# Performance work log

Hardware: AMD Instinct MI355X
Metric: run time of the kernel (lower is better)

## Reference

```python
import jax, jax.numpy as jnp
import numpy as np


def setup_inputs() -> dict:
    key = jax.random.key(0)
    k1, k2, k3 = jax.random.split(key, 3)
    B, Cin, Cout, K, H, W = 4, 64, 64, 3, 160, 160
    inputs = jax.random.normal(k1, (B, Cin, H, W), dtype=jnp.float32)
    # fractional dilation rates in [1, 3]
    rate_map = 1.0 + 2.0 * jax.random.uniform(k2, (B, 1, H, W), dtype=jnp.float32)
    # xavier-uniform-ish init
    limit = float(np.sqrt(6.0 / (Cin * K * K + Cout * K * K)))
    weight = jax.random.uniform(k3, (Cout, Cin, K, K), dtype=jnp.float32,
                                minval=-limit, maxval=limit)
    bias = jnp.zeros((Cout,), dtype=jnp.float32)
    return {"inputs": inputs, "weight": weight, "rate_map": rate_map,
            "bias": bias, "stride_h": 1, "stride_w": 1}


def _pdconv2d(inputs, weight, rate_map, bias, stride_h, stride_w):
    """Perspective (fractional, per-pixel) dilated conv with same padding.

    For each output pixel, the KxK taps are placed at center + offset*rate,
    where rate comes from rate_map and may be fractional -> bilinear sampling
    with zeros outside the image.
    """
    B, C, H, W = inputs.shape
    O, _, K, _ = weight.shape
    HO = (H + stride_h - 1) // stride_h
    WO = (W + stride_w - 1) // stride_w

    rate = rate_map[:, 0, ::stride_h, ::stride_w]  # [B,HO,WO]
    cy = (jnp.arange(HO) * stride_h).astype(jnp.float32)
    cx = (jnp.arange(WO) * stride_w).astype(jnp.float32)
    off = jnp.arange(K, dtype=jnp.float32) - (K - 1) / 2.0  # centered taps

    # sampling coords [B,HO,WO,K,K]
    sy = cy[None, :, None, None, None] + off[None, None, None, :, None] * rate[:, :, :, None, None]
    sx = cx[None, None, :, None, None] + off[None, None, None, None, :] * rate[:, :, :, None, None]
    sy = jnp.broadcast_to(sy, (B, HO, WO, K, K))
    sx = jnpp = jnp.broadcast_to(sx, (B, HO, WO, K, K))
    sx = jnp_p = sx  # no-op alias (keeps names clear)

    y0 = jnp.floor(sy)
    x0 = jnp.floor(sx)
    wy = sy - y0  # bilinear weights
    wx = sx - x0
    y0i = y0.astype(jnp.int32)
    x0i = x0.astype(jnp.int32)

    img = inputs.reshape(B, C, H * W)

    def gather(idx):  # idx [B,HO,WO,K,K] -> [B,C,HO,WO,K,K]
        return jax.vmap(lambda im, ix: jnp.take(im, ix, axis=-1))(img, idx)

    acc = jnp.zeros((B, C, HO, WO, K, K), dtype=inputs.dtype)
    corners = [(0, 0, (1 - wy) * (1 - wx)), (0, 1, (1 - wy) * wx),
               (1, 0, wy * (1 - wx)), (1, 1, wy * wx)]
    for dy, dx, cw in corners:
        yy = y0i + dy
        xx = x0i + dx
        valid = (yy >= 0) & (yy < H) & (xx >= 0) & (xx < W)
        idx = jnp.clip(yy, 0, H - 1) * W + jnp.clip(xx, 0, W - 1)
        w = (cw * valid.astype(inputs.dtype))[:, None]  # [B,1,HO,WO,K,K]
        acc = acc + gather(idx) * w

    # [B,C,HO,WO,K,K] x [O,C,K,K] -> [B,O,HO,WO]
    out = jnp.einsum('bchwkl,ockl->bohw', acc, weight)
    return out + bias[None, :, None, None]


def reference(inputs, weight, rate_map, bias, stride_h, stride_w):
    return _pdconv2d(inputs, weight, rate_map, bias, stride_h, stride_w)
```

## Files before the change

kernel.cpp:

```cpp
#include <hip/hip_runtime.h>
#include <hip/hip_bf16.h>

#define NB   4
#define CIN  64
#define COUT 64
#define HH   160
#define WW   160
#define HW   (HH * WW)

#define RT   8
#define CT   22
#define RS   72
#define RSB  (RS * 2)
#define HIN_SHORTS (RT * CT * RS)

typedef __attribute__((ext_vector_type(8))) short bf16x8;
typedef __attribute__((ext_vector_type(4))) float f32x4;
typedef __attribute__((ext_vector_type(2))) float f32x2;
typedef __attribute__((ext_vector_type(4))) unsigned int u32x4;

static __device__ __forceinline__ short f2bf(float v) {
    return __builtin_bit_cast(short, __float2bfloat16(v));
}

__global__ void wtf_kernel(const float* __restrict__ w, short* __restrict__ wtf) {
    int i = blockIdx.x * 256 + threadIdx.x;
    if (i < 36864) {
        const int j  = i & 7;
        const int l  = (i >> 3) & 63;
        const int mt = (i >> 9) & 3;
        const int ks = (i >> 11) & 1;
        const int t  = i >> 12;
        const int o  = 16 * mt + (l & 15);
        const int c  = 32 * ks + 8 * (l >> 4) + j;
        wtf[i] = f2bf(w[(o * CIN + c) * 9 + t]);
    }
}

__global__ __launch_bounds__(256) void tin_kernel(const float* __restrict__ in,
                                                  short* __restrict__ tin) {
    const int cpx = gridDim.x >> 3;
    const int wb  = (blockIdx.x & 7) * cpx + (blockIdx.x >> 3);
    const int gid = wb * 256 + threadIdx.x;
    if (gid >= NB * HW) return;
    const int b  = gid / HW;
    const int hw = gid - b * HW;
    const float* src = in + (size_t)b * CIN * HW + hw;
    short* dst = tin + (size_t)gid * CIN;
#pragma unroll
    for (int chunk = 0; chunk < 4; ++chunk) {
        union { u32x4 v; short s[8]; } p0, p1;
#pragma unroll
        for (int cc = 0; cc < 8; ++cc)
            p0.s[cc] = f2bf(src[(size_t)(chunk * 16 + cc) * HW]);
#pragma unroll
        for (int cc = 0; cc < 8; ++cc)
            p1.s[cc] = f2bf(src[(size_t)(chunk * 16 + 8 + cc) * HW]);
        *(u32x4*)(dst + chunk * 16)     = p0.v;
        *(u32x4*)(dst + chunk * 16 + 8) = p1.v;
    }
}

static __device__ __forceinline__ void consume_tap(
    const u32x4 v00, const u32x4 v01, const u32x4 v10, const u32x4 v11,
    const float c00, const float c01, const float c10, const float c11,
    const bf16x8 wf0, const bf16x8 wf1, const bf16x8 wf2, const bf16x8 wf3,
    f32x4 acc[4])
{
    union { bf16x8 v; unsigned u[4]; } pf;
#pragma unroll
    for (int wd = 0; wd < 4; ++wd) {
        f32x2 s;
        {
            const unsigned u0 = v00[wd];
            const f32x2 xv = { __builtin_bit_cast(float, u0 << 16),
                               __builtin_bit_cast(float, u0 & 0xffff0000u) };
            s = c00 * xv;
        }
        {
            const unsigned u0 = v01[wd];
            const f32x2 xv = { __builtin_bit_cast(float, u0 << 16),
                               __builtin_bit_cast(float, u0 & 0xffff0000u) };
            s += c01 * xv;
        }
        {
            const unsigned u0 = v10[wd];
            const f32x2 xv = { __builtin_bit_cast(float, u0 << 16),
                               __builtin_bit_cast(float, u0 & 0xffff0000u) };
            s += c10 * xv;
        }
        {
            const unsigned u0 = v11[wd];
            const f32x2 xv = { __builtin_bit_cast(float, u0 << 16),
                               __builtin_bit_cast(float, u0 & 0xffff0000u) };
            s += c11 * xv;
        }
        unsigned r;
        asm("v_cvt_pk_bf16_f32 %0, %1, %2" : "=v"(r) : "v"(s.x), "v"(s.y));
        pf.u[wd] = r;
    }
    acc[0] = __builtin_amdgcn_mfma_f32_16x16x32_bf16(wf0, pf.v, acc[0], 0, 0, 0);
    acc[1] = __builtin_amdgcn_mfma_f32_16x16x32_bf16(wf1, pf.v, acc[1], 0, 0, 0);
    acc[2] = __builtin_amdgcn_mfma_f32_16x16x32_bf16(wf2, pf.v, acc[2], 0, 0, 0);
    acc[3] = __builtin_amdgcn_mfma_f32_16x16x32_bf16(wf3, pf.v, acc[3], 0, 0, 0);
}

__global__ __launch_bounds__(256, 4) void pdconv_tile_kernel(
    const short* __restrict__ tin,
    const short* __restrict__ wtf,
    const float* __restrict__ rate_map,
    const float* __restrict__ bias,
    float* __restrict__ out)
{
    __shared__ short hin[HIN_SHORTS];
    __shared__ float red[2][64][17];

    const int tid  = threadIdx.x;
    const int wave = tid >> 6;
    const int lane = tid & 63;
    const int px   = lane & 15;
    const int g    = lane >> 4;
    const int r    = wave >> 1;
    const int th   = wave & 1;

    const int cpx = gridDim.x >> 3;
    const int bid = (blockIdx.x & 7) * cpx + (blockIdx.x >> 3);

    const int b   = bid / 800;
    const int rem = bid - b * 800;
    const int rr  = rem / 10;
    const int cc  = rem - rr * 10;
    const int oy  = 2 * rr - 3;
    const int ox  = 16 * cc - 3;

    const short* ib = tin + (size_t)b * HW * CIN;
#pragma unroll
    for (int it = 0; it < 6; ++it) {
        const int idx = it * 256 + tid;
        if (idx < RT * CT * 8) {
            const int rec = idx >> 3;
            const int cp  = idx & 7;
            const int ty  = rec / CT;
            const int tx  = rec - ty * CT;
            const int gy  = min(max(oy + ty, 0), HH - 1);
            const int gx  = min(max(ox + tx, 0), WW - 1);
            const u32x4 v = *(const u32x4*)(ib + ((size_t)gy * WW + gx) * CIN + cp * 8);
            *(u32x4*)(hin + rec * RS + cp * 8) = v;
        }
    }

    const int row = 2 * rr + r;
    const int x   = 16 * cc + px;
    const float rate = rate_map[b * HW + row * WW + x];
    const float fy = (float)row, fx = (float)x;

    float wy0v[3], wy1v[3];  int ryb[3];
#pragma unroll
    for (int ky = 0; ky < 3; ++ky) {
        const float sy  = fy + (float)(ky - 1) * rate;
        const float y0f = floorf(sy);
        const float wy  = sy - y0f;
        const int   y0  = (int)y0f;
        const float vy0 = (y0 >= 0 && y0 < HH) ? 1.0f : 0.0f;
        const float vy1 = (y0 + 1 >= 0 && y0 + 1 < HH) ? 1.0f : 0.0f;
        wy0v[ky] = (1.0f - wy) * vy0;
        wy1v[ky] = wy * vy1;
        ryb[ky]  = (y0 - oy) * (CT * RSB);
    }
    float wx0v[3], wx1v[3];  int txb[3];
#pragma unroll
    for (int kx = 0; kx < 3; ++kx) {
        const float sx  = fx + (float)(kx - 1) * rate;
        const float x0f = floorf(sx);
        const float wx  = sx - x0f;
        const int   x0  = (int)x0f;
        const float vx0 = (x0 >= 0 && x0 < WW) ? 1.0f : 0.0f;
        const float vx1 = (x0 + 1 >= 0 && x0 + 1 < WW) ? 1.0f : 0.0f;
        wx0v[kx] = (1.0f - wx) * vx0;
        wx1v[kx] = wx * vx1;
        txb[kx]  = (x0 - ox) * RSB;
    }

    const int chan_off = 32 * th + 8 * g;

    const short* wtb = wtf + lane * 8;

    f32x4 acc[4];
#pragma unroll
    for (int mt = 0; mt < 4; ++mt) acc[mt] = (f32x4){0.f, 0.f, 0.f, 0.f};

    __syncthreads();

#define DO_TAP(T) do {                                                       \
    const int ky = (T) / 3, kx = (T) - 3 * ((T) / 3);         \
    const float c00 = wy0v[ky] * wx0v[kx];                                   \
    const float c01 = wy0v[ky] * wx1v[kx];                                   \
    const float c10 = wy1v[ky] * wx0v[kx];                                   \
    const float c11 = wy1v[ky] * wx1v[kx];                                   \
    const short* hk = (const short*)((const char*)hin + ryb[ky] + txb[kx])   \
                      + chan_off;                                            \
    const u32x4 v00 = *(const u32x4*)(hk);                                   \
    const u32x4 v01 = *(const u32x4*)(hk + RS);                              \
    const u32x4 v10 = *(const u32x4*)(hk + CT * RS);                         \
    const u32x4 v11 = *(const u32x4*)(hk + (CT + 1) * RS);                   \
    const short* wb = wtb + (size_t)(((T) * 2 + th) * 4) * 512;              \
    const bf16x8 wf0 = *(const bf16x8*)(wb);                                 \
    const bf16x8 wf1 = *(const bf16x8*)(wb + 512);                           \
    const bf16x8 wf2 = *(const bf16x8*)(wb + 1024);                          \
    const bf16x8 wf3 = *(const bf16x8*)(wb + 1536);                          \
    consume_tap(v00, v01, v10, v11, c00, c01, c10, c11,                      \
                wf0, wf1, wf2, wf3, acc);                                    \
} while (0)

    DO_TAP(0); DO_TAP(1); DO_TAP(2); DO_TAP(3); DO_TAP(4);
    DO_TAP(5); DO_TAP(6); DO_TAP(7); DO_TAP(8);
#undef DO_TAP

    if (th == 1) {
#pragma unroll
        for (int mt = 0; mt < 4; ++mt)
#pragma unroll
            for (int j = 0; j < 4; ++j)
                red[r][lane][4 * mt + j] = acc[mt][j];
    }
    __syncthreads();
    if (th == 0) {
        float* op = out + (size_t)b * COUT * HW + row * WW + 16 * cc + px;
#pragma unroll
        for (int mt = 0; mt < 4; ++mt) {
            const f32x4 bv = *(const f32x4*)(bias + 16 * mt + 4 * g);
#pragma unroll
            for (int j = 0; j < 4; ++j) {
                const int o = 16 * mt + 4 * g + j;
                op[(size_t)o * HW] = acc[mt][j] + red[r][lane][4 * mt + j]
                                   + bv[j];
            }
        }
    }
}

__global__ void wt2_kernel(const float* __restrict__ w, short* __restrict__ wt2) {
    int i = blockIdx.x * 256 + threadIdx.x;
    if (i < 9 * COUT * CIN) {
        int c = i & 63, o = (i >> 6) & 63, t = i >> 12;
        wt2[i] = f2bf(w[(o * CIN + c) * 9 + t]);
    }
}

__global__ __launch_bounds__(256) void pdconv_mfma_kernel(
    const float* __restrict__ in, const short* __restrict__ wt2,
    const float* __restrict__ rate_map, const float* __restrict__ bias,
    float* __restrict__ out)
{
    const int tid = threadIdx.x, wave = tid >> 6, lane = tid & 63;
    const int px = lane & 15, g = lane >> 4;
    const int cpx = gridDim.x >> 3;
    const int bid = (blockIdx.x & 7) * cpx + (blockIdx.x >> 3);
    const int base = bid * 64 + wave * 16;
    const int b = base / HW, pix0 = base - b * HW;
    const int y = pix0 / WW, x0 = pix0 - y * WW, x = x0 + px;
    const float rate = rate_map[base + px];
    const float fy = (float)y, fx = (float)x;
    f32x4 acc[4];
#pragma unroll
    for (int mt = 0; mt < 4; ++mt) acc[mt] = (f32x4){0.f, 0.f, 0.f, 0.f};
    const float* img  = in + (size_t)b * CIN * HW;
    const float* imgg = img + (size_t)g * 8 * HW;
#pragma unroll 1
    for (int t = 0; t < 9; ++t) {
        const int ky = t / 3, kx = t - 3 * ky;
        const float sy = fy + (float)(ky - 1) * rate;
        const float sx = fx + (float)(kx - 1) * rate;
        const float y0f = floorf(sy), x0f = floorf(sx);
        const float wy = sy - y0f, wx = sx - x0f;
        const int y0 = (int)y0f, x0i = (int)x0f, y1 = y0 + 1, x1 = x0i + 1;
        const float omwy = 1.0f - wy, omwx = 1.0f - wx;
        const float vy0 = (y0 >= 0 && y0 < HH) ? 1.0f : 0.0f;
        const float vy1 = (y1 >= 0 && y1 < HH) ? 1.0f : 0.0f;
        const float vx0 = (x0i >= 0 && x0i < WW) ? 1.0f : 0.0f;
        const float vx1 = (x1 >= 0 && x1 < WW) ? 1.0f : 0.0f;
        const float c00 = omwy * omwx * vy0 * vx0, c01 = omwy * wx * vy0 * vx1;
        const float c10 = wy * omwx * vy1 * vx0,  c11 = wy * wx * vy1 * vx1;
        const int cy0 = min(max(y0, 0), HH - 1), cy1 = min(max(y1, 0), HH - 1);
        const int cx0 = min(max(x0i, 0), WW - 1), cx1 = min(max(x1, 0), WW - 1);
        const int i00 = cy0 * WW + cx0, i01 = cy0 * WW + cx1;
        const int i10 = cy1 * WW + cx0, i11 = cy1 * WW + cx1;
#pragma unroll
        for (int ks = 0; ks < 2; ++ks) {
            bf16x8 wf[4];
#pragma unroll
            for (int mt = 0; mt < 4; ++mt)
                wf[mt] = *(const bf16x8*)(wt2 +
                          ((t * COUT + 16 * mt + px) * CIN + 32 * ks + 8 * g));
            float a[8];
#pragma unroll
            for (int j = 0; j < 8; ++j) {
                const float* ch = imgg + (size_t)(32 * ks + j) * HW;
                a[j] = c00 * ch[i00] + c01 * ch[i01] + c10 * ch[i10] + c11 * ch[i11];
            }
            union { bf16x8 v; short s[8]; } pf;
#pragma unroll
            for (int j = 0; j < 8; ++j) pf.s[j] = f2bf(a[j]);
#pragma unroll
            for (int mt = 0; mt < 4; ++mt)
                acc[mt] = __builtin_amdgcn_mfma_f32_16x16x32_bf16(
                              wf[mt], pf.v, acc[mt], 0, 0, 0);
        }
    }
    float* op = out + (size_t)b * COUT * HW + pix0 + px;
#pragma unroll
    for (int mt = 0; mt < 4; ++mt)
#pragma unroll
        for (int r = 0; r < 4; ++r) {
            const int o = 16 * mt + 4 * g + r;
            op[(size_t)o * HW] = acc[mt][r] + bias[o];
        }
}

extern "C" void kernel_launch(void* const* d_in, const int* in_sizes, int n_in,
                              void* d_out, int out_size, void* d_ws, size_t ws_size,
                              hipStream_t stream) {
    (void)in_sizes; (void)n_in; (void)out_size;
    const float* in   = (const float*)d_in[0];
    const float* w    = (const float*)d_in[1];
    const float* rm   = (const float*)d_in[2];
    const float* bias = (const float*)d_in[3];
    float* out = (float*)d_out;

    const size_t WTF_BYTES = 36864 * sizeof(short);
    const size_t TIN_BYTES = (size_t)NB * HW * CIN * sizeof(short);

    if (ws_size >= WTF_BYTES + TIN_BYTES) {
        short* wtf = (short*)d_ws;
        short* tin = (short*)((char*)d_ws + WTF_BYTES);
        hipLaunchKernelGGL(wtf_kernel, dim3(144), dim3(256), 0, stream, w, wtf);
        hipLaunchKernelGGL(tin_kernel, dim3((NB * HW) / 256), dim3(256),
                           0, stream, in, tin);
        const int nblocks = NB * 80 * 10;
        hipLaunchKernelGGL(pdconv_tile_kernel, dim3(nblocks), dim3(256), 0,
                           stream, tin, wtf, rm, bias, out);
    } else {
        short* wt2 = (short*)d_ws;
        hipLaunchKernelGGL(wt2_kernel, dim3(144), dim3(256), 0, stream, w, wt2);
        hipLaunchKernelGGL(pdconv_mfma_kernel, dim3((NB * HW) / 64), dim3(256),
                           0, stream, in, wt2, rm, bias, out);
    }
}
```

Baseline: 47.66 us.

## Fuse NCHW-to-NHWC bf16 transpose into tile kernel's halo load

```diff
diff --git a/kernel.cpp b/kernel.cpp
--- a/kernel.cpp
+++ b/kernel.cpp
@@ -37,30 +37,6 @@
     }
 }
 
-__global__ __launch_bounds__(256) void tin_kernel(const float* __restrict__ in,
-                                                  short* __restrict__ tin) {
-    const int cpx = gridDim.x >> 3;
-    const int wb  = (blockIdx.x & 7) * cpx + (blockIdx.x >> 3);
-    const int gid = wb * 256 + threadIdx.x;
-    if (gid >= NB * HW) return;
-    const int b  = gid / HW;
-    const int hw = gid - b * HW;
-    const float* src = in + (size_t)b * CIN * HW + hw;
-    short* dst = tin + (size_t)gid * CIN;
-#pragma unroll
-    for (int chunk = 0; chunk < 4; ++chunk) {
-        union { u32x4 v; short s[8]; } p0, p1;
-#pragma unroll
-        for (int cc = 0; cc < 8; ++cc)
-            p0.s[cc] = f2bf(src[(size_t)(chunk * 16 + cc) * HW]);
-#pragma unroll
-        for (int cc = 0; cc < 8; ++cc)
-            p1.s[cc] = f2bf(src[(size_t)(chunk * 16 + 8 + cc) * HW]);
-        *(u32x4*)(dst + chunk * 16)     = p0.v;
-        *(u32x4*)(dst + chunk * 16 + 8) = p1.v;
-    }
-}
-
 static __device__ __forceinline__ void consume_tap(
     const u32x4 v00, const u32x4 v01, const u32x4 v10, const u32x4 v11,
     const float c00, const float c01, const float c10, const float c11,
@@ -106,7 +82,7 @@
 }
 
 __global__ __launch_bounds__(256, 4) void pdconv_tile_kernel(
-    const short* __restrict__ tin,
+    const float* __restrict__ in,
     const short* __restrict__ wtf,
     const float* __restrict__ rate_map,
     const float* __restrict__ bias,
@@ -133,20 +109,16 @@
     const int oy  = 2 * rr - 3;
     const int ox  = 16 * cc - 3;
 
-    const short* ib = tin + (size_t)b * HW * CIN;
-#pragma unroll
-    for (int it = 0; it < 6; ++it) {
-        const int idx = it * 256 + tid;
-        if (idx < RT * CT * 8) {
-            const int rec = idx >> 3;
-            const int cp  = idx & 7;
-            const int ty  = rec / CT;
-            const int tx  = rec - ty * CT;
-            const int gy  = min(max(oy + ty, 0), HH - 1);
-            const int gx  = min(max(ox + tx, 0), WW - 1);
-            const u32x4 v = *(const u32x4*)(ib + ((size_t)gy * WW + gx) * CIN + cp * 8);
-            *(u32x4*)(hin + rec * RS + cp * 8) = v;
-        }
+    if (tid < RT * CT) {
+        const int ty = tid / CT;
+        const int tx = tid - ty * CT;
+        const int gy = min(max(oy + ty, 0), HH - 1);
+        const int gx = min(max(ox + tx, 0), WW - 1);
+        const float* src = in + (size_t)b * CIN * HW + gy * WW + gx;
+        short* dst = hin + tid * RS;
+#pragma unroll 16
+        for (int c = 0; c < CIN; ++c)
+            dst[c] = f2bf(src[(size_t)c * HW]);
     }
 
     const int row = 2 * rr + r;
@@ -328,17 +300,13 @@
     float* out = (float*)d_out;
 
     const size_t WTF_BYTES = 36864 * sizeof(short);
-    const size_t TIN_BYTES = (size_t)NB * HW * CIN * sizeof(short);
-
-    if (ws_size >= WTF_BYTES + TIN_BYTES) {
+
+    if (ws_size >= WTF_BYTES) {
         short* wtf = (short*)d_ws;
-        short* tin = (short*)((char*)d_ws + WTF_BYTES);
         hipLaunchKernelGGL(wtf_kernel, dim3(144), dim3(256), 0, stream, w, wtf);
-        hipLaunchKernelGGL(tin_kernel, dim3((NB * HW) / 256), dim3(256),
-                           0, stream, in, tin);
         const int nblocks = NB * 80 * 10;
         hipLaunchKernelGGL(pdconv_tile_kernel, dim3(nblocks), dim3(256), 0,
-                           stream, tin, wtf, rm, bias, out);
+                           stream, in, wtf, rm, bias, out);
     } else {
         short* wt2 = (short*)d_ws;
         hipLaunchKernelGGL(wt2_kernel, dim3(144), dim3(256), 0, stream, w, wt2);
```

Result: faster. 43.42 us (-8.9%).
